# Performance work log

Measured on AMD Instinct MI355X. Metric: run time of the kernel, lower is better.

## Reference

```python
import jax, jax.numpy as jnp
import numpy as np
from jax import lax

# ---- ConvBlock config (matches init_kwargs) ----
IN_CH, OUT_CH, K, MB = 64, 128, 3, 8
P = OUT_CH // MB            # 16 block-rows
Q = (IN_CH * K * K) // MB   # 72 block-cols (64*9=576, divisible by 8)
BN_EPS = 1e-5
ACT_THRES = 6.0


def setup_inputs() -> dict:
    key = jax.random.key(0)
    k1, k2, k3, k4 = jax.random.split(key, 4)
    x = jax.random.normal(k1, (32, IN_CH, 56, 56), dtype=jnp.float32)
    # block-decomposed MZI weight: [p, q, mb, mb]
    fan_in = IN_CH * K * K
    w_blocks = jax.random.normal(k2, (P, Q, MB, MB), dtype=jnp.float32) * (1.0 / np.sqrt(fan_in))
    gamma = jax.random.uniform(k3, (OUT_CH,), dtype=jnp.float32, minval=0.5, maxval=1.5)
    beta = jax.random.normal(k4, (OUT_CH,), dtype=jnp.float32) * 0.1
    return {"x": x, "w_blocks": w_blocks, "gamma": gamma, "beta": beta}


def _assemble_weight(w_blocks):
    # [p, q, mb, mb] -> dense [p*mb, q*mb] -> crop -> [O, I, K, K]
    p, q, mb, _ = w_blocks.shape
    w = jnp.transpose(w_blocks, (0, 2, 1, 3)).reshape(p * mb, q * mb)
    w = w[:OUT_CH, : IN_CH * K * K]
    return w.reshape(OUT_CH, IN_CH, K, K)


def reference(x, w_blocks, gamma, beta):
    # MZIBlockConv2d, weight mode, w_bit=in_bit=16 => quantizers are identity,
    # photodetect=False => plain real-valued conv with block-assembled weight.
    w = _assemble_weight(w_blocks)
    y = lax.conv_general_dilated(
        x, w,
        window_strides=(1, 1),
        padding=((1, 1), (1, 1)),
        dimension_numbers=("NCHW", "OIHW", "NCHW"),
    )
    # BatchNorm2d in training mode: batch statistics over (N, H, W), biased var
    mean = jnp.mean(y, axis=(0, 2, 3))
    var = jnp.var(y, axis=(0, 2, 3))
    inv = gamma / jnp.sqrt(var + BN_EPS)
    y = (y - mean[None, :, None, None]) * inv[None, :, None, None] + beta[None, :, None, None]
    # ReLUN(6): clipped ReLU
    return jnp.clip(y, 0.0, ACT_THRES)
```

## Files before the change

kernel.cpp:

```cpp
#include <hip/hip_runtime.h>

#define NB    32
#define CIN   64
#define COUT  128
#define HH    56
#define WW    56
#define HP    58
#define NPIX  (NB*HH*WW)
#define BN_EPSF 1e-5f
#define NXPAD (NB*CIN*HP*HP)

typedef __bf16 bf16x8 __attribute__((ext_vector_type(8)));
typedef float  f32x4  __attribute__((ext_vector_type(4)));

__global__ __launch_bounds__(256) void prep(
    const float* __restrict__ x, const float* __restrict__ wb,
    __bf16* __restrict__ xpad, __bf16* __restrict__ whi, float* __restrict__ stats)
{
    int idx = blockIdx.x * 256 + threadIdx.x;
    if (idx < NXPAD) {
        int wp = idx % HP, r = idx / HP;
        int hp = r % HP, ci = r / HP;
        __bf16 v = (__bf16)0.0f;
        if (hp >= 1 && hp <= HH && wp >= 1 && wp <= WW)
            v = (__bf16)x[(ci * HH + (hp - 1)) * WW + (wp - 1)];
        xpad[idx] = v;
        return;
    }
    idx -= NXPAD;
    if (idx < 576 * 128) {
        int col = idx >> 7, oc = idx & 127;
        int p = oc >> 3, i = oc & 7, q = col >> 3, j = col & 7;
        float v = wb[((p * 72 + q) * 8 + i) * 8 + j];
        int ic = col / 9, tap = col % 9;
        int dst = ((tap * 2 + (ic >> 5)) * 128 + oc) * 32 + (ic & 31);
        whi[dst] = (__bf16)v;
        return;
    }
    idx -= 576 * 128;
    if (idx < 256) stats[idx] = 0.0f;
}

__global__ __launch_bounds__(256, 4) void conv_mfma(
    const __bf16* __restrict__ xpad, const __bf16* __restrict__ whi,
    float* __restrict__ y, float* __restrict__ gsum, float* __restrict__ gsq)
{
    __shared__ __bf16 xs[100 * 64];

    int b = blockIdx.x;
    int ocb = b & 1;
    int tile = b >> 1;
    int n = tile / 49, t = tile % 49;
    int h0 = (t / 7) * 8, w0 = (t % 7) * 8;
    int tid  = threadIdx.x;
    int lane = tid & 63, wid = tid >> 6;
    int l15 = lane & 15, l4 = lane >> 4;
    int oc0 = ocb * 64 + wid * 16;

    int woff = (oc0 + l15) * 32 + l4 * 8;
#define BLOAD(i) const bf16x8 B##i = *(const bf16x8*)&whi[(i) * 4096 + woff]
    BLOAD(0);  BLOAD(1);  BLOAD(2);  BLOAD(3);  BLOAD(4);  BLOAD(5);
    BLOAD(6);  BLOAD(7);  BLOAD(8);  BLOAD(9);  BLOAD(10); BLOAD(11);
    BLOAD(12); BLOAD(13); BLOAD(14); BLOAD(15); BLOAD(16); BLOAD(17);
#undef BLOAD

    const __bf16* xn = xpad + n * CIN * HP * HP;
    for (int u = tid; u < 800; u += 256) {
        int c = u / 100, px = u - c * 100;
        int r = px / 10, cc = px - r * 10;
        const __bf16* src = xn + (c * 8) * (HP * HP) + (h0 + r) * HP + (w0 + cc);
        bf16x8 hv;
        #pragma unroll
        for (int j = 0; j < 8; ++j) hv[j] = src[j * HP * HP];
        *(bf16x8*)&xs[px * 64 + ((c ^ (px & 7)) * 8)] = hv;
    }
    __syncthreads();

    f32x4 acc0 = {}, acc1 = {}, acc2 = {}, acc3 = {};
    int rb0 = (l15 >> 3) * 10 + (l15 & 7);

#define KS1(BI, TOFF, C0, MT, ACC) { \
        int R  = rb0 + (MT) * 20 + (TOFF); \
        int ae = R * 64 + (((C0) ^ (R & 7)) * 8); \
        bf16x8 a = *(const bf16x8*)&xs[ae]; \
        ACC = __builtin_amdgcn_mfma_f32_16x16x32_bf16(a, BI, ACC, 0, 0, 0); }
#define KS(BI, TOFF, HALF) { \
        const int c0 = (HALF) * 4 + l4; \
        KS1(BI, TOFF, c0, 0, acc0) KS1(BI, TOFF, c0, 1, acc1) \
        KS1(BI, TOFF, c0, 2, acc2) KS1(BI, TOFF, c0, 3, acc3) }

    KS(B0,  0, 0) KS(B1,  0, 1) KS(B2,  1, 0) KS(B3,  1, 1)
    KS(B4,  2, 0) KS(B5,  2, 1) KS(B6, 10, 0) KS(B7, 10, 1)
    KS(B8, 11, 0) KS(B9, 11, 1) KS(B10,12, 0) KS(B11,12, 1)
    KS(B12,20, 0) KS(B13,20, 1) KS(B14,21, 0) KS(B15,21, 1)
    KS(B16,22, 0) KS(B17,22, 1)
#undef KS
#undef KS1

    float* yn = y + n * COUT * HH * WW;
    int pyb = l4 >> 1;
    int gwo = w0 + (l4 & 1) * 4;
    int oc  = oc0 + l15;
    {
        int gh0 = h0 + pyb;
        *(float4*)&yn[(oc * HH + gh0    ) * WW + gwo] = *(float4*)&acc0;
        *(float4*)&yn[(oc * HH + gh0 + 2) * WW + gwo] = *(float4*)&acc1;
        *(float4*)&yn[(oc * HH + gh0 + 4) * WW + gwo] = *(float4*)&acc2;
        *(float4*)&yn[(oc * HH + gh0 + 6) * WW + gwo] = *(float4*)&acc3;
    }

    float* red = (float*)xs;
    float s = 0.0f, sq = 0.0f;
    #pragma unroll
    for (int r = 0; r < 4; ++r) {
        float v0 = acc0[r], v1 = acc1[r], v2 = acc2[r], v3 = acc3[r];
        s  += v0 + v1 + v2 + v3;
        sq += v0 * v0 + v1 * v1 + v2 * v2 + v3 * v3;
    }
    s  += __shfl_xor(s, 16, 64);  s  += __shfl_xor(s, 32, 64);
    sq += __shfl_xor(sq, 16, 64); sq += __shfl_xor(sq, 32, 64);
    __syncthreads();
    if (l4 == 0) {
        int o = wid * 16 + l15;
        red[o] = s; red[64 + o] = sq;
    }
    __syncthreads();
    if (tid < 64) {
        atomicAdd(&gsum[ocb * 64 + tid], red[tid]);
        atomicAdd(&gsq [ocb * 64 + tid], red[64 + tid]);
    }
}

__global__ __launch_bounds__(256) void bn_apply(float* __restrict__ y,
        const float* __restrict__ gsum, const float* __restrict__ gsq,
        const float* __restrict__ gamma, const float* __restrict__ beta)
{
    __shared__ float ssc[128], ssh[128];
    int tid = threadIdx.x;
    if (tid < 128) {
        float mean = gsum[tid] * (1.0f / NPIX);
        float var  = gsq[tid]  * (1.0f / NPIX) - mean * mean;
        float inv  = gamma[tid] / sqrtf(var + BN_EPSF);
        ssc[tid] = inv;
        ssh[tid] = beta[tid] - mean * inv;
    }
    __syncthreads();

    const int total4 = NB * COUT * HH * WW / 4;
    int idx = blockIdx.x * blockDim.x + tid;
    int stride = gridDim.x * blockDim.x;
    for (int i4 = idx; i4 < total4; i4 += stride) {
        int c = (i4 / 784) & 127;
        float sc = ssc[c], sh = ssh[c];
        float4 v = ((float4*)y)[i4];
        v.x = fminf(fmaxf(fmaf(v.x, sc, sh), 0.0f), 6.0f);
        v.y = fminf(fmaxf(fmaf(v.y, sc, sh), 0.0f), 6.0f);
        v.z = fminf(fmaxf(fmaf(v.z, sc, sh), 0.0f), 6.0f);
        v.w = fminf(fmaxf(fmaf(v.w, sc, sh), 0.0f), 6.0f);
        ((float4*)y)[i4] = v;
    }
}

extern "C" void kernel_launch(void* const* d_in, const int* in_sizes, int n_in,
                              void* d_out, int out_size, void* d_ws, size_t ws_size,
                              hipStream_t stream) {
    const float* x     = (const float*)d_in[0];
    const float* wb    = (const float*)d_in[1];
    const float* gamma = (const float*)d_in[2];
    const float* beta  = (const float*)d_in[3];
    float* y = (float*)d_out;

    __bf16* xpad  = (__bf16*)d_ws;
    __bf16* whi   = xpad + NXPAD;
    float*  stats = (float*)(whi + 73728);
    float*  gsum  = stats;
    float*  gsq   = stats + 128;

    int prep_grid = (NXPAD + 576 * 128 + 256 + 255) / 256;
    prep<<<prep_grid, 256, 0, stream>>>(x, wb, xpad, whi, stats);
    conv_mfma<<<NB * 49 * 2, 256, 0, stream>>>(xpad, whi, y, gsum, gsq);
    bn_apply<<<2048, 256, 0, stream>>>(y, gsum, gsq, gamma, beta);
}
```

Measured before the change: 185.7 us.

## Fuse input padding and bf16 conversion into conv tile load

Drops the separate padded bf16 copy of x that the prep kernel used to build. The conv kernel now reads fp32 x directly, bounds-checks the halo and converts to bf16 while filling shared memory. This saves writing and re-reading a padded intermediate of about 13 MB. The cost is reading fp32 (twice the bytes) with redundant halo reads across tiles, and launch bounds drop from 4 to 2 blocks per CU, which may change register allocation and occupancy.

```diff
diff --git a/kernel.cpp b/kernel.cpp
--- a/kernel.cpp
+++ b/kernel.cpp
@@ -5,29 +5,16 @@
 #define COUT  128
 #define HH    56
 #define WW    56
-#define HP    58
 #define NPIX  (NB*HH*WW)
 #define BN_EPSF 1e-5f
-#define NXPAD (NB*CIN*HP*HP)
 
 typedef __bf16 bf16x8 __attribute__((ext_vector_type(8)));
 typedef float  f32x4  __attribute__((ext_vector_type(4)));
 
 __global__ __launch_bounds__(256) void prep(
-    const float* __restrict__ x, const float* __restrict__ wb,
-    __bf16* __restrict__ xpad, __bf16* __restrict__ whi, float* __restrict__ stats)
+    const float* __restrict__ wb, __bf16* __restrict__ whi, float* __restrict__ stats)
 {
     int idx = blockIdx.x * 256 + threadIdx.x;
-    if (idx < NXPAD) {
-        int wp = idx % HP, r = idx / HP;
-        int hp = r % HP, ci = r / HP;
-        __bf16 v = (__bf16)0.0f;
-        if (hp >= 1 && hp <= HH && wp >= 1 && wp <= WW)
-            v = (__bf16)x[(ci * HH + (hp - 1)) * WW + (wp - 1)];
-        xpad[idx] = v;
-        return;
-    }
-    idx -= NXPAD;
     if (idx < 576 * 128) {
         int col = idx >> 7, oc = idx & 127;
         int p = oc >> 3, i = oc & 7, q = col >> 3, j = col & 7;
@@ -41,8 +28,8 @@
     if (idx < 256) stats[idx] = 0.0f;
 }
 
-__global__ __launch_bounds__(256, 4) void conv_mfma(
-    const __bf16* __restrict__ xpad, const __bf16* __restrict__ whi,
+__global__ __launch_bounds__(256, 2) void conv_mfma(
+    const float* __restrict__ x, const __bf16* __restrict__ whi,
     float* __restrict__ y, float* __restrict__ gsum, float* __restrict__ gsq)
 {
     __shared__ __bf16 xs[100 * 64];
@@ -64,14 +51,19 @@
     BLOAD(12); BLOAD(13); BLOAD(14); BLOAD(15); BLOAD(16); BLOAD(17);
 #undef BLOAD
 
-    const __bf16* xn = xpad + n * CIN * HP * HP;
+    const float* xn = x + n * CIN * HH * WW;
     for (int u = tid; u < 800; u += 256) {
         int c = u / 100, px = u - c * 100;
         int r = px / 10, cc = px - r * 10;
-        const __bf16* src = xn + (c * 8) * (HP * HP) + (h0 + r) * HP + (w0 + cc);
+        int gh = h0 - 1 + r, gw = w0 - 1 + cc;
+        bool ok = ((unsigned)gh < 56u) & ((unsigned)gw < 56u);
+        const float* src = xn + (c * 8) * (HH * WW) + gh * WW + gw;
         bf16x8 hv;
         #pragma unroll
-        for (int j = 0; j < 8; ++j) hv[j] = src[j * HP * HP];
+        for (int j = 0; j < 8; ++j) {
+            float v = ok ? src[j * HH * WW] : 0.0f;
+            hv[j] = (__bf16)v;
+        }
         *(bf16x8*)&xs[px * 64 + ((c ^ (px & 7)) * 8)] = hv;
     }
     __syncthreads();
@@ -170,14 +162,13 @@
     const float* beta  = (const float*)d_in[3];
     float* y = (float*)d_out;
 
-    __bf16* xpad  = (__bf16*)d_ws;
-    __bf16* whi   = xpad + NXPAD;
+    __bf16* whi   = (__bf16*)d_ws;
     float*  stats = (float*)(whi + 73728);
     float*  gsum  = stats;
     float*  gsq   = stats + 128;
 
-    int prep_grid = (NXPAD + 576 * 128 + 256 + 255) / 256;
-    prep<<<prep_grid, 256, 0, stream>>>(x, wb, xpad, whi, stats);
-    conv_mfma<<<NB * 49 * 2, 256, 0, stream>>>(xpad, whi, y, gsum, gsq);
+    int prep_grid = (576 * 128 + 256 + 255) / 256;
+    prep<<<prep_grid, 256, 0, stream>>>(wb, whi, stats);
+    conv_mfma<<<NB * 49 * 2, 256, 0, stream>>>(x, whi, y, gsum, gsq);
     bn_apply<<<2048, 256, 0, stream>>>(y, gsum, gsq, gamma, beta);
 }
```

Result: slower. 193.6 us (+4.2%).
